# Optimization experiments

Hardware: AMD Instinct MI355X
Metric: run time of the kernel (lower is better)

## Reference

```python
import jax, jax.numpy as jnp
import numpy as np
from jax import lax

NEG = -1e16  # value used by masked_fill in the original
DN = ('NCHW', 'OIHW', 'NCHW')


def _time_block(X, w1, b1, w2, b2, w3, b3):
    # X: [B, N, T, C] -> conv over time with kernel (1,3), VALID -> [B, N, T-2, O]
    x = jnp.transpose(X, (0, 3, 1, 2))  # [B, C, N, T]
    conv = lambda w, b: lax.conv_general_dilated(x, w, (1, 1), 'VALID', dimension_numbers=DN) + b[None, :, None, None]
    temp = conv(w1, b1) + jax.nn.sigmoid(conv(w2, b2))
    out = jax.nn.relu(temp + conv(w3, b3))
    return jnp.transpose(out, (0, 2, 3, 1))  # [B, N, T-2, O]


def _gat_single(x, graph, W, b):
    # x: [B, N, C]; W: [D, C]; b: [D]
    h = jnp.einsum('bnc,dc->bnd', x, W)
    s = jnp.einsum('bnd,bmd->bnm', h, h) * graph[None]
    s = jnp.where(s == 0, NEG, s)
    a = jax.nn.softmax(s, axis=-1)
    return jnp.einsum('bnm,bmd->bnd', a, h) + b


def _gat_multihead(x, graph, Wh, bh):
    # x: [B, N, C]; Wh: [H, D, C]; bh: [H, D] -> [B, N, H*D] (head-major concat, matching torch.cat)
    h = jnp.einsum('bnc,hdc->bhnd', x, Wh)
    s = jnp.einsum('bhnd,bhmd->bhnm', h, h) * graph[None, None]
    s = jnp.where(s == 0, NEG, s)
    a = jax.nn.softmax(s, axis=-1)
    o = jnp.einsum('bhnm,bhmd->bhnd', a, h) + bh[None, :, None, :]
    B, H, N, D = o.shape
    return jnp.transpose(o, (0, 2, 1, 3)).reshape(B, N, H * D)


def setup_inputs() -> dict:
    key = jax.random.key(0)
    ks = jax.random.split(key, 12)
    B, N, T, C = 2, 4096, 5, 192
    hid, out_c, H = 64, 64, 4
    inp = {
        'flow': jax.random.normal(ks[0], (B, N, T, C), jnp.float32),
        'graph': jax.random.randint(ks[1], (N, N), 0, 2).astype(jnp.float32),
        'tb_w1': jax.random.normal(ks[2], (hid, C, 1, 3), jnp.float32) * 0.1,
        'tb_b1': jax.random.normal(ks[3], (hid,), jnp.float32) * 0.1,
        'tb_w2': jax.random.normal(ks[4], (hid, C, 1, 3), jnp.float32) * 0.1,
        'tb_b2': jax.random.normal(ks[5], (hid,), jnp.float32) * 0.1,
        'tb_w3': jax.random.normal(ks[6], (hid, C, 1, 3), jnp.float32) * 0.1,
        'tb_b3': jax.random.normal(ks[7], (hid,), jnp.float32) * 0.1,
        'Wh': jax.random.normal(ks[8], (H, hid, C), jnp.float32) * 0.1,
        'bh': jax.random.normal(ks[9], (H, hid), jnp.float32) * 0.1,
        'Wo': jax.random.normal(ks[10], (out_c, hid * H), jnp.float32) * 0.1,
        'bo': jax.random.normal(ks[11], (out_c,), jnp.float32) * 0.1,
    }
    return inp


def reference(flow, graph, tb_w1, tb_b1, tb_w2, tb_b2, tb_w3, tb_b3, Wh, bh, Wo, bo):
    B, N = flow.shape[0], flow.shape[1]
    t1 = _time_block(flow, tb_w1, tb_b1, tb_w2, tb_b2, tb_w3, tb_b3)  # [B, N, T-2, hid]
    x = t1.reshape(B, N, -1)  # [B, N, (T-2)*hid]
    x = jax.nn.leaky_relu(_gat_multihead(x, graph, Wh, bh), negative_slope=0.01)
    x = jax.nn.leaky_relu(_gat_single(x, graph, Wo, bo), negative_slope=0.01)
    return x[:, :, None, :]  # [B, N, 1, out_c]
```

## Files before the change

### kernel.cpp

```cpp
#include <hip/hip_runtime.h>
#include <math.h>

#define N_NODES 4096

typedef unsigned short u16;
typedef unsigned int u32;

typedef __attribute__((ext_vector_type(8))) short bfrag;
typedef __attribute__((ext_vector_type(4))) float f4;

__device__ __forceinline__ u16 f2bf(float x) {
    union { float f; u32 u; } v; v.f = x;
    u32 r = (v.u + 0x7FFFu + ((v.u >> 16) & 1u)) >> 16;
    return (u16)r;
}
__device__ __forceinline__ float bf2f(u16 b) {
    union { float f; u32 u; } v; v.u = ((u32)b) << 16; return v.f;
}
__device__ __forceinline__ u32 cvtpk(float a, float b) {
    u32 r;
    asm("v_cvt_pk_bf16_f32 %0, %1, %2" : "=v"(r) : "v"(a), "v"(b));
    return r;
}
__device__ __forceinline__ float u2f(u32 u) {
    union { u32 u; float f; } v; v.u = u; return v.f;
}
__device__ __forceinline__ float fexp2(float x) {
    float r;
    asm("v_exp_f32 %0, %1" : "=v"(r) : "v"(x));
    return r;
}

#define LOG2E 1.4426950408889634f

__global__ __launch_bounds__(256) void wprep_kernel(
    const float* __restrict__ w1, const float* __restrict__ w2,
    const float* __restrict__ w3,
    u16* __restrict__ w_hi, u16* __restrict__ w_mid, u16* __restrict__ w_lo)
{
    int idx = blockIdx.x * 256 + threadIdx.x;
    if (idx >= 192 * 576) return;
    int col = idx / 576, k = idx % 576;
    int conv = col >> 6, o = col & 63;
    int kk = k / 192, c = k % 192;
    const float* w = (conv == 0) ? w1 : (conv == 1 ? w2 : w3);
    float v = w[(o * 192 + c) * 3 + kk];
    u16 h = f2bf(v);   float r1 = v - bf2f(h);
    u16 m = f2bf(r1);  float r2 = r1 - bf2f(m);
    u16 lo = f2bf(r2);
    int kc = k >> 6, rem = k & 63, j = rem >> 3, e = rem & 7;
    int pos = col * 576 + kc * 64 + ((j ^ (col & 7)) << 3) + e;
    w_hi[pos] = h;
    w_mid[pos] = m;
    w_lo[pos] = lo;
}

__global__ __launch_bounds__(512) void timeblock_mfma_kernel(
    const float* __restrict__ flow,
    const u16* __restrict__ w_hi, const u16* __restrict__ w_mid,
    const u16* __restrict__ w_lo,
    const float* __restrict__ b1, const float* __restrict__ b2,
    const float* __restrict__ b3, float* __restrict__ x1)
{
    __shared__ __align__(16) u16 As[3][128 * 64];
    __shared__ __align__(16) u16 Bs[3][192 * 64];

    const int tid = threadIdx.x;
    const int wv = tid >> 6, l = tid & 63;
    const int ln15 = l & 15, ln16 = l >> 4;
    const int wr = wv >> 1, wc = wv & 1;
    const int nodebase = blockIdx.x * 128;
    const int t = blockIdx.y;

    f4 acc[2][6];
#pragma unroll
    for (int rq = 0; rq < 2; ++rq)
#pragma unroll
        for (int nt = 0; nt < 6; ++nt) {
            acc[rq][nt][0] = 0.f; acc[rq][nt][1] = 0.f;
            acc[rq][nt][2] = 0.f; acc[rq][nt][3] = 0.f;
        }

    for (int kc = 0; kc < 9; ++kc) {
        __syncthreads();

#pragma unroll
        for (int u = tid; u < 1024; u += 512) {
            int r = u >> 3, j = u & 7;
            const float* srcp = flow + (size_t)(nodebase + r) * 960 + t * 192 + kc * 64 + j * 8;
            float4 f0 = *(const float4*)srcp;
            float4 f1 = *(const float4*)(srcp + 4);
            float fv[8] = { f0.x, f0.y, f0.z, f0.w, f1.x, f1.y, f1.z, f1.w };
            union { uint4 q; u16 a[8]; } uh, um, ul;
#pragma unroll
            for (int e = 0; e < 8; ++e) {
                u16 h = f2bf(fv[e]);   float r1 = fv[e] - bf2f(h);
                u16 m = f2bf(r1);      float r2 = r1 - bf2f(m);
                uh.a[e] = h; um.a[e] = m; ul.a[e] = f2bf(r2);
            }
            int pos = r * 64 + ((j ^ (r & 7)) << 3);
            *(uint4*)&As[0][pos] = uh.q;
            *(uint4*)&As[1][pos] = um.q;
            *(uint4*)&As[2][pos] = ul.q;
        }

#pragma unroll
        for (int arr = 0; arr < 3; ++arr) {
            const u16* wsrc = (arr == 0) ? w_hi : (arr == 1 ? w_mid : w_lo);
#pragma unroll
            for (int i = 0; i < 3; ++i) {
                int colg = wv * 24 + i * 8;
                const u16* srcp = wsrc + (size_t)(colg + (l >> 3)) * 576 + kc * 64 + (l & 7) * 8;
                u16* dstp = &Bs[arr][colg * 64];
                __builtin_amdgcn_global_load_lds(
                    (const __attribute__((address_space(1))) u32*)srcp,
                    (__attribute__((address_space(3))) u32*)dstp, 16, 0, 0);
            }
        }

        __syncthreads();

        bfrag af[2][3][2];
#pragma unroll
        for (int rq = 0; rq < 2; ++rq) {
            int arow = wr * 32 + rq * 16 + ln15;
#pragma unroll
            for (int ks = 0; ks < 2; ++ks) {
                int idx = arow * 64 + (((ks * 4 + ln16) ^ (arow & 7)) << 3);
                af[rq][0][ks] = *(const bfrag*)&As[0][idx];
                af[rq][1][ks] = *(const bfrag*)&As[1][idx];
                af[rq][2][ks] = *(const bfrag*)&As[2][idx];
            }
        }

#pragma unroll
        for (int cv = 0; cv < 3; ++cv) {
#pragma unroll
            for (int ntj = 0; ntj < 2; ++ntj) {
                int col = cv * 64 + wc * 32 + ntj * 16 + ln15;
                int nt = cv * 2 + ntj;
#pragma unroll
                for (int ks = 0; ks < 2; ++ks) {
                    int idx = col * 64 + (((ks * 4 + ln16) ^ (col & 7)) << 3);
                    bfrag bh = *(const bfrag*)&Bs[0][idx];
                    bfrag bm = *(const bfrag*)&Bs[1][idx];
                    bfrag bl = *(const bfrag*)&Bs[2][idx];
#pragma unroll
                    for (int rq = 0; rq < 2; ++rq) {
                        f4 a = acc[rq][nt];
                        a = __builtin_amdgcn_mfma_f32_16x16x32_bf16(af[rq][0][ks], bh, a, 0, 0, 0);
                        a = __builtin_amdgcn_mfma_f32_16x16x32_bf16(af[rq][0][ks], bm, a, 0, 0, 0);
                        a = __builtin_amdgcn_mfma_f32_16x16x32_bf16(af[rq][1][ks], bh, a, 0, 0, 0);
                        a = __builtin_amdgcn_mfma_f32_16x16x32_bf16(af[rq][0][ks], bl, a, 0, 0, 0);
                        a = __builtin_amdgcn_mfma_f32_16x16x32_bf16(af[rq][2][ks], bh, a, 0, 0, 0);
                        a = __builtin_amdgcn_mfma_f32_16x16x32_bf16(af[rq][1][ks], bm, a, 0, 0, 0);
                        acc[rq][nt] = a;
                    }
                }
            }
        }
    }

#pragma unroll
    for (int rq = 0; rq < 2; ++rq) {
#pragma unroll
        for (int ntj = 0; ntj < 2; ++ntj) {
            int o = wc * 32 + ntj * 16 + ln15;
            float bb1 = b1[o], bb2 = b2[o], bb3 = b3[o];
#pragma unroll
            for (int rg = 0; rg < 4; ++rg) {
                int node = nodebase + wr * 32 + rq * 16 + ln16 * 4 + rg;
                float c1 = acc[rq][0 * 2 + ntj][rg] + bb1;
                float c2 = acc[rq][1 * 2 + ntj][rg] + bb2;
                float c3 = acc[rq][2 * 2 + ntj][rg] + bb3;
                float sg = 1.0f / (1.0f + __expf(-c2));
                float v = c1 + sg + c3;
                x1[(size_t)node * 192 + t * 64 + o] = v > 0.f ? v : 0.f;
            }
        }
    }
}

__global__ __launch_bounds__(256) void linear64_split_kernel(
    const float* __restrict__ in, const float* __restrict__ W,
    u16* __restrict__ h_hi, u16* __restrict__ h_lo,
    u16* __restrict__ hTb_hi, u16* __restrict__ hTb_lo,
    int C, int H)
{
    __shared__ float xs[64][68];
    __shared__ float wsm[64][68];
    const int tid = threadIdx.x;
    const int g = blockIdx.y;
    const int rowbase = blockIdx.x * 64;
    const int rgrp = tid >> 4, cgrp = tid & 15;

    float acc[4][4] = {};
    for (int c0 = 0; c0 < C; c0 += 64) {
        __syncthreads();
        for (int i = tid; i < 4096; i += 256) {
            int r = i >> 6, cc = i & 63;
            xs[r][cc]  = in[(size_t)(rowbase + r) * C + c0 + cc];
            wsm[r][cc] = W[(size_t)(g * 64 + r) * C + c0 + cc];
        }
        __syncthreads();
        for (int cc = 0; cc < 64; cc += 4) {
            float4 xv[4], wv[4];
#pragma unroll
            for (int i = 0; i < 4; ++i)
                xv[i] = *reinterpret_cast<const float4*>(&xs[4 * rgrp + i][cc]);
#pragma unroll
            for (int j = 0; j < 4; ++j)
                wv[j] = *reinterpret_cast<const float4*>(&wsm[4 * cgrp + j][cc]);
#pragma unroll
            for (int i = 0; i < 4; ++i) {
#pragma unroll
                for (int j = 0; j < 4; ++j) {
                    acc[i][j] += xv[i].x * wv[j].x + xv[i].y * wv[j].y
                               + xv[i].z * wv[j].z + xv[i].w * wv[j].w;
                }
            }
        }
    }

    u16 hi[4][4], lo[4][4];
#pragma unroll
    for (int i = 0; i < 4; ++i)
#pragma unroll
        for (int j = 0; j < 4; ++j) {
            float a = acc[i][j];
            u16 h = f2bf(a);
            hi[i][j] = h;
            lo[i][j] = f2bf(a - bf2f(h));
        }

    const int b = rowbase >> 12;
    const size_t mapb = (size_t)(b * H + g) * (4096 * 64);

#pragma unroll
    for (int i = 0; i < 4; ++i) {
        int n = (rowbase & 4095) + 4 * rgrp + i;
        ushort4 vh = { hi[i][0], hi[i][1], hi[i][2], hi[i][3] };
        ushort4 vl = { lo[i][0], lo[i][1], lo[i][2], lo[i][3] };
        *(ushort4*)&h_hi[mapb + (size_t)n * 64 + 4 * cgrp] = vh;
        *(ushort4*)&h_lo[mapb + (size_t)n * 64 + 4 * cgrp] = vl;
    }
    {
        int n0 = (rowbase & 4095) + 4 * rgrp;
        size_t tb = mapb + ((size_t)(n0 >> 6) * 64) * 64;
#pragma unroll
        for (int j = 0; j < 4; ++j) {
            int d = 4 * cgrp + j;
            ushort4 vh = { hi[0][j], hi[1][j], hi[2][j], hi[3][j] };
            ushort4 vl = { lo[0][j], lo[1][j], lo[2][j], lo[3][j] };
            *(ushort4*)&hTb_hi[tb + (size_t)d * 64 + (n0 & 63)] = vh;
            *(ushort4*)&hTb_lo[tb + (size_t)d * 64 + (n0 & 63)] = vl;
        }
    }
}

__global__ __launch_bounds__(256) void flash_mfma_kernel(
    const u16* __restrict__ h_hi, const u16* __restrict__ h_lo,
    const u16* __restrict__ hTb_hi, const u16* __restrict__ hTb_lo,
    const float* __restrict__ graph, const float* __restrict__ bias,
    float* __restrict__ out, int H, int rstride,
    int ntiles, int nch, int mode, float* __restrict__ pO, float* __restrict__ pml)
{
    __shared__ __align__(16) u16 hcs[2][4][4096];

    const int tid = threadIdx.x;
    const int wv = tid >> 6;
    const int l = tid & 63;
    const int ln15 = l & 15, ln16 = l >> 4;
    const int bx = blockIdx.x;
    const int by = bx / nch;
    const int chunk = bx - by * nch;
    const int t0 = chunk * ntiles;
    const int bb = by / H, head = by - bb * H;
    const size_t mapb = (size_t)by * (4096 * 64);
    const int rowbase = blockIdx.y * 64;

    const int arow = rowbase + wv * 16 + ln15;
    bfrag ahi[2], alo[2];
#pragma unroll
    for (int ks = 0; ks < 2; ++ks) {
        ahi[ks] = *(const bfrag*)(h_hi + mapb + (size_t)arow * 64 + ks * 32 + ln16 * 8);
        alo[ks] = *(const bfrag*)(h_lo + mapb + (size_t)arow * 64 + ks * 32 + ln16 * 8);
    }

    const u16* gA = (wv == 0 ? h_hi : wv == 1 ? h_lo : wv == 2 ? hTb_hi : hTb_lo) + mapb;
    const int lrow = l >> 3;
    const int stoff = lrow * 64 + (((l & 7) ^ lrow) << 3);

#define STAGE(T, BUF)                                                          \
    {                                                                          \
        const u16* srcp = gA + (size_t)(T) * 4096 + stoff;                     \
        u16* dstp = &hcs[BUF][wv][0];                                          \
        _Pragma("unroll")                                                      \
        for (int i_ = 0; i_ < 8; ++i_)                                         \
            __builtin_amdgcn_global_load_lds(                                  \
                (const __attribute__((address_space(1))) u32*)(srcp + i_ * 512), \
                (__attribute__((address_space(3))) u32*)(dstp + i_ * 512),     \
                16, 0, 0);                                                     \
    }

    const float* grow = graph + (size_t)(rowbase + wv * 16 + ln15) * 4096 + ln16 * 4;

    float m_ = -3.0e38f, l_ = 0.f;
    f4 acco[4];
#pragma unroll
    for (int i = 0; i < 4; ++i) {
        acco[i][0] = 0.f; acco[i][1] = 0.f; acco[i][2] = 0.f; acco[i][3] = 0.f;
    }

    STAGE(t0, 0);
    float4 grC[4], grN[4];
#pragma unroll
    for (int cb = 0; cb < 4; ++cb)
        grC[cb] = *(const float4*)(grow + (size_t)t0 * 64 + cb * 16);

    const int srcA = ln15 + ((((ln16 << 1)) & 3) << 4);
    const int srcB = ln15 + ((((ln16 << 1) + 1) & 3) << 4);
    const bool hi2 = (ln16 & 2) != 0;

    for (int tt = 0; tt < ntiles; ++tt) {
        const int t = t0 + tt;
        const int cur = tt & 1;

        __syncthreads();

        if (tt + 1 < ntiles) {
            STAGE(t + 1, cur ^ 1);
#pragma unroll
            for (int cb = 0; cb < 4; ++cb)
                grN[cb] = *(const float4*)(grow + (size_t)(t + 1) * 64 + cb * 16);
        }

        __builtin_amdgcn_s_setprio(1);
        f4 accs[4];
#pragma unroll
        for (int cb = 0; cb < 4; ++cb) {
            f4 a; a[0] = 0.f; a[1] = 0.f; a[2] = 0.f; a[3] = 0.f;
#pragma unroll
            for (int ks = 0; ks < 2; ++ks) {
                int c = cb * 16 + ln15;
                int idx = c * 64 + (((ks * 4 + ln16) * 8) ^ ((c & 7) << 3));
                bfrag bhi = *(const bfrag*)&hcs[cur][0][idx];
                bfrag blo = *(const bfrag*)&hcs[cur][1][idx];
                a = __builtin_amdgcn_mfma_f32_16x16x32_bf16(bhi, ahi[ks], a, 0, 0, 0);
                a = __builtin_amdgcn_mfma_f32_16x16x32_bf16(bhi, alo[ks], a, 0, 0, 0);
                a = __builtin_amdgcn_mfma_f32_16x16x32_bf16(blo, ahi[ks], a, 0, 0, 0);
            }
            accs[cb] = a;
        }
        __builtin_amdgcn_s_setprio(0);

        float p[4][4];
#pragma unroll
        for (int cb = 0; cb < 4; ++cb) {
            p[cb][0] = accs[cb][0] + fmaf(grC[cb].x, 1e16f, -1e16f);
            p[cb][1] = accs[cb][1] + fmaf(grC[cb].y, 1e16f, -1e16f);
            p[cb][2] = accs[cb][2] + fmaf(grC[cb].z, 1e16f, -1e16f);
            p[cb][3] = accs[cb][3] + fmaf(grC[cb].w, 1e16f, -1e16f);
        }

        float tm = fmaxf(fmaxf(p[0][0], p[0][1]), fmaxf(p[0][2], p[0][3]));
#pragma unroll
        for (int cb = 1; cb < 4; ++cb)
            tm = fmaxf(tm, fmaxf(fmaxf(p[cb][0], p[cb][1]), fmaxf(p[cb][2], p[cb][3])));
        tm = fmaxf(tm, __shfl_xor(tm, 16));
        tm = fmaxf(tm, __shfl_xor(tm, 32));

        const bool anyup = __any(tm > m_);
        float mn, corr;
        if (anyup) {
            mn = fmaxf(m_, tm);
            corr = fexp2((m_ - mn) * LOG2E);
        } else {
            mn = m_;
            corr = 1.0f;
        }
        const float c0 = -mn * LOG2E;

        float rs = 0.f;
#pragma unroll
        for (int cb = 0; cb < 4; ++cb) {
            p[cb][0] = fexp2(fmaf(p[cb][0], LOG2E, c0));
            p[cb][1] = fexp2(fmaf(p[cb][1], LOG2E, c0));
            p[cb][2] = fexp2(fmaf(p[cb][2], LOG2E, c0));
            p[cb][3] = fexp2(fmaf(p[cb][3], LOG2E, c0));
            rs += (p[cb][0] + p[cb][1]) + (p[cb][2] + p[cb][3]);
        }
        rs += __shfl_xor(rs, 16);
        rs += __shfl_xor(rs, 32);
        l_ = l_ * corr + rs;
        m_ = mn;

        if (anyup) {
            float corr4[4];
#pragma unroll
            for (int rg = 0; rg < 4; ++rg)
                corr4[rg] = __shfl(corr, ln16 * 4 + rg);
#pragma unroll
            for (int nb = 0; nb < 4; ++nb) {
                acco[nb][0] *= corr4[0]; acco[nb][1] *= corr4[1];
                acco[nb][2] *= corr4[2]; acco[nb][3] *= corr4[3];
            }
        }

        u32 Uh[4][2], Ul[4][2];
#pragma unroll
        for (int cb = 0; cb < 4; ++cb) {
            u32 uh0 = cvtpk(p[cb][0], p[cb][1]);
            u32 uh1 = cvtpk(p[cb][2], p[cb][3]);
            float h0 = u2f(uh0 << 16), h1 = u2f(uh0 & 0xffff0000u);
            float h2 = u2f(uh1 << 16), h3 = u2f(uh1 & 0xffff0000u);
            Uh[cb][0] = uh0; Uh[cb][1] = uh1;
            Ul[cb][0] = cvtpk(p[cb][0] - h0, p[cb][1] - h1);
            Ul[cb][1] = cvtpk(p[cb][2] - h2, p[cb][3] - h3);
        }

        bfrag pfh[2], pfl[2];
#pragma unroll
        for (int ks = 0; ks < 2; ++ks) {
            u32 w0a = (u32)__shfl((int)Uh[2 * ks + 0][0], srcA);
            u32 w0b = (u32)__shfl((int)Uh[2 * ks + 1][0], srcA);
            u32 w1a = (u32)__shfl((int)Uh[2 * ks + 0][1], srcA);
            u32 w1b = (u32)__shfl((int)Uh[2 * ks + 1][1], srcA);
            u32 w2a = (u32)__shfl((int)Uh[2 * ks + 0][0], srcB);
            u32 w2b = (u32)__shfl((int)Uh[2 * ks + 1][0], srcB);
            u32 w3a = (u32)__shfl((int)Uh[2 * ks + 0][1], srcB);
            u32 w3b = (u32)__shfl((int)Uh[2 * ks + 1][1], srcB);
            union { uint4 q; bfrag f; } ch;
            ch.q.x = hi2 ? w0b : w0a; ch.q.y = hi2 ? w1b : w1a;
            ch.q.z = hi2 ? w2b : w2a; ch.q.w = hi2 ? w3b : w3a;
            pfh[ks] = ch.f;

            u32 v0a = (u32)__shfl((int)Ul[2 * ks + 0][0], srcA);
            u32 v0b = (u32)__shfl((int)Ul[2 * ks + 1][0], srcA);
            u32 v1a = (u32)__shfl((int)Ul[2 * ks + 0][1], srcA);
            u32 v1b = (u32)__shfl((int)Ul[2 * ks + 1][1], srcA);
            u32 v2a = (u32)__shfl((int)Ul[2 * ks + 0][0], srcB);
            u32 v2b = (u32)__shfl((int)Ul[2 * ks + 1][0], srcB);
            u32 v3a = (u32)__shfl((int)Ul[2 * ks + 0][1], srcB);
            u32 v3b = (u32)__shfl((int)Ul[2 * ks + 1][1], srcB);
            union { uint4 q; bfrag f; } cl;
            cl.q.x = hi2 ? v0b : v0a; cl.q.y = hi2 ? v1b : v1a;
            cl.q.z = hi2 ? v2b : v2a; cl.q.w = hi2 ? v3b : v3a;
            pfl[ks] = cl.f;
        }

        __builtin_amdgcn_s_setprio(1);
#pragma unroll
        for (int nb = 0; nb < 4; ++nb) {
#pragma unroll
            for (int ks = 0; ks < 2; ++ks) {
                int nr = nb * 16 + ln15;
                int idx = nr * 64 + (((ks * 4 + ln16) * 8) ^ ((nr & 7) << 3));
                bfrag vhi = *(const bfrag*)&hcs[cur][2][idx];
                bfrag vlo = *(const bfrag*)&hcs[cur][3][idx];
                acco[nb] = __builtin_amdgcn_mfma_f32_16x16x32_bf16(pfh[ks], vhi, acco[nb], 0, 0, 0);
                acco[nb] = __builtin_amdgcn_mfma_f32_16x16x32_bf16(pfh[ks], vlo, acco[nb], 0, 0, 0);
                acco[nb] = __builtin_amdgcn_mfma_f32_16x16x32_bf16(pfl[ks], vhi, acco[nb], 0, 0, 0);
            }
        }
        __builtin_amdgcn_s_setprio(0);

        if (tt + 1 < ntiles) {
#pragma unroll
            for (int cb = 0; cb < 4; ++cb)
                grC[cb] = grN[cb];
        }
    }
#undef STAGE

    if (mode == 0) {
        float l4[4];
#pragma unroll
        for (int rg = 0; rg < 4; ++rg)
            l4[rg] = __shfl(l_, ln16 * 4 + rg);

        const float* bv = bias + head * 64;
#pragma unroll
        for (int rg = 0; rg < 4; ++rg) {
            int row = rowbase + wv * 16 + ln16 * 4 + rg;
            float inv = 1.0f / l4[rg];
#pragma unroll
            for (int nb = 0; nb < 4; ++nb) {
                float v = acco[nb][rg] * inv + bv[nb * 16 + ln15];
                v = v > 0.f ? v : 0.01f * v;
                out[(size_t)(bb * N_NODES + row) * rstride + head * 64 + nb * 16 + ln15] = v;
            }
        }
    } else {
        int row = rowbase + wv * 16 + ln15;
        if (ln16 == 0) {
            size_t mi = (((size_t)(by * nch + chunk)) * 4096 + row) * 2;
            pml[mi] = m_;
            pml[mi + 1] = l_;
        }
#pragma unroll
        for (int rg = 0; rg < 4; ++rg) {
            int row2 = rowbase + wv * 16 + ln16 * 4 + rg;
            size_t ob = (((size_t)(by * nch + chunk)) * 4096 + row2) * 64;
#pragma unroll
            for (int nb = 0; nb < 4; ++nb)
                pO[ob + nb * 16 + ln15] = acco[nb][rg];
        }
    }
}

__global__ __launch_bounds__(256) void merge_kernel(
    const float* __restrict__ pO, const float* __restrict__ pml,
    const float* __restrict__ bias, float* __restrict__ out)
{
    int idx = blockIdx.x * 256 + threadIdx.x;
    int feat = idx & 63;
    int row = (idx >> 6) & 4095;
    int map = idx >> 18;

    float mv[4], lv[4];
    float M = -3.0e38f;
#pragma unroll
    for (int c = 0; c < 4; ++c) {
        size_t mi = (((size_t)map * 4 + c) * 4096 + row) * 2;
        mv[c] = pml[mi];
        lv[c] = pml[mi + 1];
        M = fmaxf(M, mv[c]);
    }
    float den = 0.f, num = 0.f;
#pragma unroll
    for (int c = 0; c < 4; ++c) {
        float e = __expf(mv[c] - M);
        den += e * lv[c];
        num += e * pO[(((size_t)map * 4 + c) * 4096 + row) * 64 + feat];
    }
    float v = num / den + bias[feat];
    v = v > 0.f ? v : 0.01f * v;
    out[((size_t)map * 4096 + row) * 64 + feat] = v;
}

extern "C" void kernel_launch(void* const* d_in, const int* in_sizes, int n_in,
                              void* d_out, int out_size, void* d_ws, size_t ws_size,
                              hipStream_t stream)
{
    const float* flow = (const float*)d_in[0];
    const float* graph = (const float*)d_in[1];
    const float* w1 = (const float*)d_in[2];
    const float* b1 = (const float*)d_in[3];
    const float* w2 = (const float*)d_in[4];
    const float* b2 = (const float*)d_in[5];
    const float* w3 = (const float*)d_in[6];
    const float* b3 = (const float*)d_in[7];
    const float* Wh = (const float*)d_in[8];
    const float* bh = (const float*)d_in[9];
    const float* Wo = (const float*)d_in[10];
    const float* bo = (const float*)d_in[11];

    char* ws = (char*)d_ws;
    u16* wc_hi  = (u16*)ws;
    u16* wc_mid = wc_hi + (size_t)192 * 576;
    u16* wc_lo  = wc_mid + (size_t)192 * 576;

    u16* h1_hi  = (u16*)ws;
    u16* h1_lo  = h1_hi + (size_t)8 * 4096 * 64;
    u16* h1T_hi = h1_lo + (size_t)8 * 4096 * 64;
    u16* h1T_lo = h1T_hi + (size_t)8 * 4096 * 64;
    u16* h2_hi  = (u16*)ws;
    u16* h2_lo  = h2_hi + (size_t)2 * 4096 * 64;
    u16* h2T_hi = h2_lo + (size_t)2 * 4096 * 64;
    u16* h2T_lo = h2T_hi + (size_t)2 * 4096 * 64;
    float* pml  = (float*)(ws + (size_t)6 * 1024 * 1024);
    float* xreg = (float*)(ws + (size_t)4 * 8 * 4096 * 64 * 2);
    float* x1 = xreg;
    float* x2 = xreg;
    float* pO = xreg;
    float* outp = (float*)d_out;

    hipLaunchKernelGGL(wprep_kernel, dim3(432), dim3(256), 0, stream,
                       w1, w2, w3, wc_hi, wc_mid, wc_lo);
    hipLaunchKernelGGL(timeblock_mfma_kernel, dim3(64, 3), dim3(512), 0, stream,
                       flow, wc_hi, wc_mid, wc_lo, b1, b2, b3, x1);
    hipLaunchKernelGGL(linear64_split_kernel, dim3(128, 4), dim3(256), 0, stream,
                       x1, Wh, h1_hi, h1_lo, h1T_hi, h1T_lo, 192, 4);
    hipLaunchKernelGGL(flash_mfma_kernel, dim3(8, 64), dim3(256), 0, stream,
                       h1_hi, h1_lo, h1T_hi, h1T_lo, graph, bh, x2, 4, 256,
                       64, 1, 0, (float*)nullptr, (float*)nullptr);
    hipLaunchKernelGGL(linear64_split_kernel, dim3(128, 1), dim3(256), 0, stream,
                       x2, Wo, h2_hi, h2_lo, h2T_hi, h2T_lo, 256, 1);
    hipLaunchKernelGGL(flash_mfma_kernel, dim3(8, 64), dim3(256), 0, stream,
                       h2_hi, h2_lo, h2T_hi, h2T_lo, graph, bo, (float*)nullptr, 1, 64,
                       16, 4, 1, pO, pml);
    hipLaunchKernelGGL(merge_kernel, dim3(2048), dim3(256), 0, stream,
                       pO, pml, bo, outp);
}
```

Before: 314.6 us.

## Stream K/V fragments directly from global memory instead of LDS staging

Removes the double-buffered LDS staging of key and value tiles (global_load_lds plus __syncthreads) and has each wave load its MFMA B-operand fragments straight from global memory into registers. It also drops the graph-row prefetch and sets launch bounds to allow four blocks per CU. The aim is to remove block-wide barriers and LDS traffic and to gain occupancy. In exchange, all four waves now fetch the same K/V data separately, relying on L1/L2 for reuse, and global latency is no longer hidden by explicit prefetching.

```diff
diff --git a/kernel.cpp b/kernel.cpp
--- a/kernel.cpp
+++ b/kernel.cpp
@@ -258,15 +258,13 @@
     }
 }
 
-__global__ __launch_bounds__(256) void flash_mfma_kernel(
+__global__ __launch_bounds__(256, 4) void flash_stream_kernel(
     const u16* __restrict__ h_hi, const u16* __restrict__ h_lo,
     const u16* __restrict__ hTb_hi, const u16* __restrict__ hTb_lo,
     const float* __restrict__ graph, const float* __restrict__ bias,
     float* __restrict__ out, int H, int rstride,
     int ntiles, int nch, int mode, float* __restrict__ pO, float* __restrict__ pml)
 {
-    __shared__ __align__(16) u16 hcs[2][4][4096];
-
     const int tid = threadIdx.x;
     const int wv = tid >> 6;
     const int l = tid & 63;
@@ -277,33 +275,23 @@
     const int t0 = chunk * ntiles;
     const int bb = by / H, head = by - bb * H;
     const size_t mapb = (size_t)by * (4096 * 64);
-    const int rowbase = blockIdx.y * 64;
-
-    const int arow = rowbase + wv * 16 + ln15;
-    bfrag ahi[2], alo[2];
+    const int rowbase = blockIdx.y * 64 + wv * 16;
+
+    const int arow = rowbase + ln15;
+    bfrag qhi[2], qlo[2];
 #pragma unroll
     for (int ks = 0; ks < 2; ++ks) {
-        ahi[ks] = *(const bfrag*)(h_hi + mapb + (size_t)arow * 64 + ks * 32 + ln16 * 8);
-        alo[ks] = *(const bfrag*)(h_lo + mapb + (size_t)arow * 64 + ks * 32 + ln16 * 8);
-    }
-
-    const u16* gA = (wv == 0 ? h_hi : wv == 1 ? h_lo : wv == 2 ? hTb_hi : hTb_lo) + mapb;
-    const int lrow = l >> 3;
-    const int stoff = lrow * 64 + (((l & 7) ^ lrow) << 3);
-
-#define STAGE(T, BUF)                                                          \
-    {                                                                          \
-        const u16* srcp = gA + (size_t)(T) * 4096 + stoff;                     \
-        u16* dstp = &hcs[BUF][wv][0];                                          \
-        _Pragma("unroll")                                                      \
-        for (int i_ = 0; i_ < 8; ++i_)                                         \
-            __builtin_amdgcn_global_load_lds(                                  \
-                (const __attribute__((address_space(1))) u32*)(srcp + i_ * 512), \
-                (__attribute__((address_space(3))) u32*)(dstp + i_ * 512),     \
-                16, 0, 0);                                                     \
-    }
-
-    const float* grow = graph + (size_t)(rowbase + wv * 16 + ln15) * 4096 + ln16 * 4;
+        qhi[ks] = *(const bfrag*)(h_hi + mapb + (size_t)arow * 64 + ks * 32 + ln16 * 8);
+        qlo[ks] = *(const bfrag*)(h_lo + mapb + (size_t)arow * 64 + ks * 32 + ln16 * 8);
+    }
+
+    const int foff = ln15 * 64 + ln16 * 8;
+    const u16* kb_hi = h_hi + mapb + foff;
+    const u16* kb_lo = h_lo + mapb + foff;
+    const u16* vb_hi = hTb_hi + mapb + foff;
+    const u16* vb_lo = hTb_lo + mapb + foff;
+
+    const float* grow = graph + (size_t)(rowbase + ln15) * 4096 + ln16 * 4;
 
     float m_ = -3.0e38f, l_ = 0.f;
     f4 acco[4];
@@ -311,12 +299,6 @@
     for (int i = 0; i < 4; ++i) {
         acco[i][0] = 0.f; acco[i][1] = 0.f; acco[i][2] = 0.f; acco[i][3] = 0.f;
     }
-
-    STAGE(t0, 0);
-    float4 grC[4], grN[4];
-#pragma unroll
-    for (int cb = 0; cb < 4; ++cb)
-        grC[cb] = *(const float4*)(grow + (size_t)t0 * 64 + cb * 16);
 
     const int srcA = ln15 + ((((ln16 << 1)) & 3) << 4);
     const int srcB = ln15 + ((((ln16 << 1) + 1) & 3) << 4);
@@ -324,32 +306,30 @@
 
     for (int tt = 0; tt < ntiles; ++tt) {
         const int t = t0 + tt;
-        const int cur = tt & 1;
-
-        __syncthreads();
-
-        if (tt + 1 < ntiles) {
-            STAGE(t + 1, cur ^ 1);
-#pragma unroll
-            for (int cb = 0; cb < 4; ++cb)
-                grN[cb] = *(const float4*)(grow + (size_t)(t + 1) * 64 + cb * 16);
-        }
+        const size_t tb = (size_t)t * 4096;
+
+        float4 grC[4];
+#pragma unroll
+        for (int cb = 0; cb < 4; ++cb)
+            grC[cb] = *(const float4*)(grow + (size_t)t * 64 + cb * 16);
 
         __builtin_amdgcn_s_setprio(1);
         f4 accs[4];
 #pragma unroll
         for (int cb = 0; cb < 4; ++cb) {
+            const u16* kh = kb_hi + tb + cb * 1024;
+            const u16* kl = kb_lo + tb + cb * 1024;
+            bfrag kh0 = *(const bfrag*)kh;
+            bfrag kh1 = *(const bfrag*)(kh + 32);
+            bfrag kl0 = *(const bfrag*)kl;
+            bfrag kl1 = *(const bfrag*)(kl + 32);
             f4 a; a[0] = 0.f; a[1] = 0.f; a[2] = 0.f; a[3] = 0.f;
-#pragma unroll
-            for (int ks = 0; ks < 2; ++ks) {
-                int c = cb * 16 + ln15;
-                int idx = c * 64 + (((ks * 4 + ln16) * 8) ^ ((c & 7) << 3));
-                bfrag bhi = *(const bfrag*)&hcs[cur][0][idx];
-                bfrag blo = *(const bfrag*)&hcs[cur][1][idx];
-                a = __builtin_amdgcn_mfma_f32_16x16x32_bf16(bhi, ahi[ks], a, 0, 0, 0);
-                a = __builtin_amdgcn_mfma_f32_16x16x32_bf16(bhi, alo[ks], a, 0, 0, 0);
-                a = __builtin_amdgcn_mfma_f32_16x16x32_bf16(blo, ahi[ks], a, 0, 0, 0);
-            }
+            a = __builtin_amdgcn_mfma_f32_16x16x32_bf16(kh0, qhi[0], a, 0, 0, 0);
+            a = __builtin_amdgcn_mfma_f32_16x16x32_bf16(kh0, qlo[0], a, 0, 0, 0);
+            a = __builtin_amdgcn_mfma_f32_16x16x32_bf16(kl0, qhi[0], a, 0, 0, 0);
+            a = __builtin_amdgcn_mfma_f32_16x16x32_bf16(kh1, qhi[1], a, 0, 0, 0);
+            a = __builtin_amdgcn_mfma_f32_16x16x32_bf16(kh1, qlo[1], a, 0, 0, 0);
+            a = __builtin_amdgcn_mfma_f32_16x16x32_bf16(kl1, qhi[1], a, 0, 0, 0);
             accs[cb] = a;
         }
         __builtin_amdgcn_s_setprio(0);
@@ -452,26 +432,21 @@
         __builtin_amdgcn_s_setprio(1);
 #pragma unroll
         for (int nb = 0; nb < 4; ++nb) {
-#pragma unroll
-            for (int ks = 0; ks < 2; ++ks) {
-                int nr = nb * 16 + ln15;
-                int idx = nr * 64 + (((ks * 4 + ln16) * 8) ^ ((nr & 7) << 3));
-                bfrag vhi = *(const bfrag*)&hcs[cur][2][idx];
-                bfrag vlo = *(const bfrag*)&hcs[cur][3][idx];
-                acco[nb] = __builtin_amdgcn_mfma_f32_16x16x32_bf16(pfh[ks], vhi, acco[nb], 0, 0, 0);
-                acco[nb] = __builtin_amdgcn_mfma_f32_16x16x32_bf16(pfh[ks], vlo, acco[nb], 0, 0, 0);
-                acco[nb] = __builtin_amdgcn_mfma_f32_16x16x32_bf16(pfl[ks], vhi, acco[nb], 0, 0, 0);
-            }
+            const u16* vh = vb_hi + tb + nb * 1024;
+            const u16* vl = vb_lo + tb + nb * 1024;
+            bfrag vh0 = *(const bfrag*)vh;
+            bfrag vh1 = *(const bfrag*)(vh + 32);
+            bfrag vl0 = *(const bfrag*)vl;
+            bfrag vl1 = *(const bfrag*)(vl + 32);
+            acco[nb] = __builtin_amdgcn_mfma_f32_16x16x32_bf16(pfh[0], vh0, acco[nb], 0, 0, 0);
+            acco[nb] = __builtin_amdgcn_mfma_f32_16x16x32_bf16(pfh[0], vl0, acco[nb], 0, 0, 0);
+            acco[nb] = __builtin_amdgcn_mfma_f32_16x16x32_bf16(pfl[0], vh0, acco[nb], 0, 0, 0);
+            acco[nb] = __builtin_amdgcn_mfma_f32_16x16x32_bf16(pfh[1], vh1, acco[nb], 0, 0, 0);
+            acco[nb] = __builtin_amdgcn_mfma_f32_16x16x32_bf16(pfh[1], vl1, acco[nb], 0, 0, 0);
+            acco[nb] = __builtin_amdgcn_mfma_f32_16x16x32_bf16(pfl[1], vh1, acco[nb], 0, 0, 0);
         }
         __builtin_amdgcn_s_setprio(0);
-
-        if (tt + 1 < ntiles) {
-#pragma unroll
-            for (int cb = 0; cb < 4; ++cb)
-                grC[cb] = grN[cb];
-        }
-    }
-#undef STAGE
+    }
 
     if (mode == 0) {
         float l4[4];
@@ -482,7 +457,7 @@
         const float* bv = bias + head * 64;
 #pragma unroll
         for (int rg = 0; rg < 4; ++rg) {
-            int row = rowbase + wv * 16 + ln16 * 4 + rg;
+            int row = rowbase + ln16 * 4 + rg;
             float inv = 1.0f / l4[rg];
 #pragma unroll
             for (int nb = 0; nb < 4; ++nb) {
@@ -492,7 +467,7 @@
             }
         }
     } else {
-        int row = rowbase + wv * 16 + ln15;
+        int row = rowbase + ln15;
         if (ln16 == 0) {
             size_t mi = (((size_t)(by * nch + chunk)) * 4096 + row) * 2;
             pml[mi] = m_;
@@ -500,7 +475,7 @@
         }
 #pragma unroll
         for (int rg = 0; rg < 4; ++rg) {
-            int row2 = rowbase + wv * 16 + ln16 * 4 + rg;
+            int row2 = rowbase + ln16 * 4 + rg;
             size_t ob = (((size_t)(by * nch + chunk)) * 4096 + row2) * 64;
 #pragma unroll
             for (int nb = 0; nb < 4; ++nb)
@@ -582,12 +557,12 @@
                        flow, wc_hi, wc_mid, wc_lo, b1, b2, b3, x1);
     hipLaunchKernelGGL(linear64_split_kernel, dim3(128, 4), dim3(256), 0, stream,
                        x1, Wh, h1_hi, h1_lo, h1T_hi, h1T_lo, 192, 4);
-    hipLaunchKernelGGL(flash_mfma_kernel, dim3(8, 64), dim3(256), 0, stream,
+    hipLaunchKernelGGL(flash_stream_kernel, dim3(8, 64), dim3(256), 0, stream,
                        h1_hi, h1_lo, h1T_hi, h1T_lo, graph, bh, x2, 4, 256,
                        64, 1, 0, (float*)nullptr, (float*)nullptr);
     hipLaunchKernelGGL(linear64_split_kernel, dim3(128, 1), dim3(256), 0, stream,
                        x2, Wo, h2_hi, h2_lo, h2T_hi, h2T_lo, 256, 1);
-    hipLaunchKernelGGL(flash_mfma_kernel, dim3(8, 64), dim3(256), 0, stream,
+    hipLaunchKernelGGL(flash_stream_kernel, dim3(8, 64), dim3(256), 0, stream,
                        h2_hi, h2_lo, h2T_hi, h2T_lo, graph, bo, (float*)nullptr, 1, 64,
                        16, 4, 1, pO, pml);
     hipLaunchKernelGGL(merge_kernel, dim3(2048), dim3(256), 0, stream,
```

Measured after the change: 742.0 us. 136% more time.

## Load V fragments directly from global memory and halve LDS staging in flash kernel

Applied to the files above, without the earlier changes.

The flash attention kernel now stages only the K hi/lo tiles through LDS, with each wave loading half of one array. The V (transposed) operand fragments are read per wave directly from global memory into registers each tile. This halves shared memory per block and adds a launch-bounds occupancy hint of 3 blocks. In exchange, each wave issues its own uncoalesced-ish global reads for V without prefetching ahead of the barrier, which raises register pressure and may expose load latency.

```diff
diff --git a/kernel.cpp b/kernel.cpp
--- a/kernel.cpp
+++ b/kernel.cpp
@@ -258,14 +258,14 @@
     }
 }
 
-__global__ __launch_bounds__(256) void flash_mfma_kernel(
+__global__ __launch_bounds__(256, 3) void flash_hybrid_kernel(
     const u16* __restrict__ h_hi, const u16* __restrict__ h_lo,
     const u16* __restrict__ hTb_hi, const u16* __restrict__ hTb_lo,
     const float* __restrict__ graph, const float* __restrict__ bias,
     float* __restrict__ out, int H, int rstride,
     int ntiles, int nch, int mode, float* __restrict__ pO, float* __restrict__ pml)
 {
-    __shared__ __align__(16) u16 hcs[2][4][4096];
+    __shared__ __align__(16) u16 hcs[2][2][4096];
 
     const int tid = threadIdx.x;
     const int wv = tid >> 6;
@@ -277,33 +277,38 @@
     const int t0 = chunk * ntiles;
     const int bb = by / H, head = by - bb * H;
     const size_t mapb = (size_t)by * (4096 * 64);
-    const int rowbase = blockIdx.y * 64;
-
-    const int arow = rowbase + wv * 16 + ln15;
-    bfrag ahi[2], alo[2];
+    const int rowbase = blockIdx.y * 64 + wv * 16;
+
+    const int arow = rowbase + ln15;
+    bfrag qhi[2], qlo[2];
 #pragma unroll
     for (int ks = 0; ks < 2; ++ks) {
-        ahi[ks] = *(const bfrag*)(h_hi + mapb + (size_t)arow * 64 + ks * 32 + ln16 * 8);
-        alo[ks] = *(const bfrag*)(h_lo + mapb + (size_t)arow * 64 + ks * 32 + ln16 * 8);
-    }
-
-    const u16* gA = (wv == 0 ? h_hi : wv == 1 ? h_lo : wv == 2 ? hTb_hi : hTb_lo) + mapb;
+        qhi[ks] = *(const bfrag*)(h_hi + mapb + (size_t)arow * 64 + ks * 32 + ln16 * 8);
+        qlo[ks] = *(const bfrag*)(h_lo + mapb + (size_t)arow * 64 + ks * 32 + ln16 * 8);
+    }
+
+    const u16* gA = (wv < 2 ? h_hi : h_lo) + mapb;
+    const int arr_ = wv >> 1, half_ = wv & 1;
     const int lrow = l >> 3;
     const int stoff = lrow * 64 + (((l & 7) ^ lrow) << 3);
 
 #define STAGE(T, BUF)                                                          \
     {                                                                          \
-        const u16* srcp = gA + (size_t)(T) * 4096 + stoff;                     \
-        u16* dstp = &hcs[BUF][wv][0];                                          \
+        const u16* srcp = gA + (size_t)(T) * 4096 + half_ * 2048 + stoff;      \
+        u16* dstp = &hcs[BUF][arr_][half_ * 2048];                             \
         _Pragma("unroll")                                                      \
-        for (int i_ = 0; i_ < 8; ++i_)                                         \
+        for (int i_ = 0; i_ < 4; ++i_)                                         \
             __builtin_amdgcn_global_load_lds(                                  \
                 (const __attribute__((address_space(1))) u32*)(srcp + i_ * 512), \
                 (__attribute__((address_space(3))) u32*)(dstp + i_ * 512),     \
                 16, 0, 0);                                                     \
     }
 
-    const float* grow = graph + (size_t)(rowbase + wv * 16 + ln15) * 4096 + ln16 * 4;
+    const int foff = ln15 * 64 + ln16 * 8;
+    const u16* vb_hi = hTb_hi + mapb + foff;
+    const u16* vb_lo = hTb_lo + mapb + foff;
+
+    const float* grow = graph + (size_t)(rowbase + ln15) * 4096 + ln16 * 4;
 
     float m_ = -3.0e38f, l_ = 0.f;
     f4 acco[4];
@@ -325,8 +330,20 @@
     for (int tt = 0; tt < ntiles; ++tt) {
         const int t = t0 + tt;
         const int cur = tt & 1;
+        const size_t tb = (size_t)t * 4096;
 
         __syncthreads();
+
+        bfrag vfh[4][2], vfl[4][2];
+#pragma unroll
+        for (int nb = 0; nb < 4; ++nb) {
+            const u16* vh = vb_hi + tb + nb * 1024;
+            const u16* vl = vb_lo + tb + nb * 1024;
+            vfh[nb][0] = *(const bfrag*)vh;
+            vfh[nb][1] = *(const bfrag*)(vh + 32);
+            vfl[nb][0] = *(const bfrag*)vl;
+            vfl[nb][1] = *(const bfrag*)(vl + 32);
+        }
 
         if (tt + 1 < ntiles) {
             STAGE(t + 1, cur ^ 1);
@@ -346,9 +363,9 @@
                 int idx = c * 64 + (((ks * 4 + ln16) * 8) ^ ((c & 7) << 3));
                 bfrag bhi = *(const bfrag*)&hcs[cur][0][idx];
                 bfrag blo = *(const bfrag*)&hcs[cur][1][idx];
-                a = __builtin_amdgcn_mfma_f32_16x16x32_bf16(bhi, ahi[ks], a, 0, 0, 0);
-                a = __builtin_amdgcn_mfma_f32_16x16x32_bf16(bhi, alo[ks], a, 0, 0, 0);
-                a = __builtin_amdgcn_mfma_f32_16x16x32_bf16(blo, ahi[ks], a, 0, 0, 0);
+                a = __builtin_amdgcn_mfma_f32_16x16x32_bf16(bhi, qhi[ks], a, 0, 0, 0);
+                a = __builtin_amdgcn_mfma_f32_16x16x32_bf16(bhi, qlo[ks], a, 0, 0, 0);
+                a = __builtin_amdgcn_mfma_f32_16x16x32_bf16(blo, qhi[ks], a, 0, 0, 0);
             }
             accs[cb] = a;
         }
@@ -452,16 +469,12 @@
         __builtin_amdgcn_s_setprio(1);
 #pragma unroll
         for (int nb = 0; nb < 4; ++nb) {
-#pragma unroll
-            for (int ks = 0; ks < 2; ++ks) {
-                int nr = nb * 16 + ln15;
-                int idx = nr * 64 + (((ks * 4 + ln16) * 8) ^ ((nr & 7) << 3));
-                bfrag vhi = *(const bfrag*)&hcs[cur][2][idx];
-                bfrag vlo = *(const bfrag*)&hcs[cur][3][idx];
-                acco[nb] = __builtin_amdgcn_mfma_f32_16x16x32_bf16(pfh[ks], vhi, acco[nb], 0, 0, 0);
-                acco[nb] = __builtin_amdgcn_mfma_f32_16x16x32_bf16(pfh[ks], vlo, acco[nb], 0, 0, 0);
-                acco[nb] = __builtin_amdgcn_mfma_f32_16x16x32_bf16(pfl[ks], vhi, acco[nb], 0, 0, 0);
-            }
+            acco[nb] = __builtin_amdgcn_mfma_f32_16x16x32_bf16(pfh[0], vfh[nb][0], acco[nb], 0, 0, 0);
+            acco[nb] = __builtin_amdgcn_mfma_f32_16x16x32_bf16(pfh[0], vfl[nb][0], acco[nb], 0, 0, 0);
+            acco[nb] = __builtin_amdgcn_mfma_f32_16x16x32_bf16(pfl[0], vfh[nb][0], acco[nb], 0, 0, 0);
+            acco[nb] = __builtin_amdgcn_mfma_f32_16x16x32_bf16(pfh[1], vfh[nb][1], acco[nb], 0, 0, 0);
+            acco[nb] = __builtin_amdgcn_mfma_f32_16x16x32_bf16(pfh[1], vfl[nb][1], acco[nb], 0, 0, 0);
+            acco[nb] = __builtin_amdgcn_mfma_f32_16x16x32_bf16(pfl[1], vfh[nb][1], acco[nb], 0, 0, 0);
         }
         __builtin_amdgcn_s_setprio(0);
 
@@ -482,7 +495,7 @@
         const float* bv = bias + head * 64;
 #pragma unroll
         for (int rg = 0; rg < 4; ++rg) {
-            int row = rowbase + wv * 16 + ln16 * 4 + rg;
+            int row = rowbase + ln16 * 4 + rg;
             float inv = 1.0f / l4[rg];
 #pragma unroll
             for (int nb = 0; nb < 4; ++nb) {
@@ -492,7 +505,7 @@
             }
         }
     } else {
-        int row = rowbase + wv * 16 + ln15;
+        int row = rowbase + ln15;
         if (ln16 == 0) {
             size_t mi = (((size_t)(by * nch + chunk)) * 4096 + row) * 2;
             pml[mi] = m_;
@@ -500,7 +513,7 @@
         }
 #pragma unroll
         for (int rg = 0; rg < 4; ++rg) {
-            int row2 = rowbase + wv * 16 + ln16 * 4 + rg;
+            int row2 = rowbase + ln16 * 4 + rg;
             size_t ob = (((size_t)(by * nch + chunk)) * 4096 + row2) * 64;
 #pragma unroll
             for (int nb = 0; nb < 4; ++nb)
@@ -582,12 +595,12 @@
                        flow, wc_hi, wc_mid, wc_lo, b1, b2, b3, x1);
     hipLaunchKernelGGL(linear64_split_kernel, dim3(128, 4), dim3(256), 0, stream,
                        x1, Wh, h1_hi, h1_lo, h1T_hi, h1T_lo, 192, 4);
-    hipLaunchKernelGGL(flash_mfma_kernel, dim3(8, 64), dim3(256), 0, stream,
+    hipLaunchKernelGGL(flash_hybrid_kernel, dim3(8, 64), dim3(256), 0, stream,
                        h1_hi, h1_lo, h1T_hi, h1T_lo, graph, bh, x2, 4, 256,
                        64, 1, 0, (float*)nullptr, (float*)nullptr);
     hipLaunchKernelGGL(linear64_split_kernel, dim3(128, 1), dim3(256), 0, stream,
                        x2, Wo, h2_hi, h2_lo, h2T_hi, h2T_lo, 256, 1);
-    hipLaunchKernelGGL(flash_mfma_kernel, dim3(8, 64), dim3(256), 0, stream,
+    hipLaunchKernelGGL(flash_hybrid_kernel, dim3(8, 64), dim3(256), 0, stream,
                        h2_hi, h2_lo, h2T_hi, h2T_lo, graph, bo, (float*)nullptr, 1, 64,
                        16, 4, 1, pO, pml);
     hipLaunchKernelGGL(merge_kernel, dim3(2048), dim3(256), 0, stream,
```

Measured after the change: 524.9 us. 1.67x slower.
